# Kernel tuning notes

Hardware: AMD Instinct MI355X
Metric: run time of the kernel (lower is better)

Reference implementation:

```python
import jax, jax.numpy as jnp
import numpy as np

USER_NUM = 200000
ITEM_NUM = 100000
EMB = 64
N_LAYERS = 2
NE_S = 3200000
NE_R = 3200000


def setup_inputs() -> dict:
    key = jax.random.key(0)
    ks = jax.random.split(key, 10)
    scale = 1.0 / np.sqrt(EMB)
    user_emb = jax.random.normal(ks[0], (USER_NUM, EMB), jnp.float32) * scale
    item_emb = jax.random.normal(ks[1], (ITEM_NUM, EMB), jnp.float32) * scale
    # torch Linear weight is [out_features, in_features] = [EMB, 2*EMB]
    W = jax.random.normal(ks[2], (N_LAYERS, EMB, 2 * EMB), jnp.float32) * (1.0 / np.sqrt(2 * EMB))
    b = jnp.zeros((N_LAYERS, EMB), jnp.float32)
    s_rows = jax.random.randint(ks[3], (NE_S,), 0, USER_NUM, jnp.int32)
    s_cols = jax.random.randint(ks[4], (NE_S,), 0, USER_NUM, jnp.int32)
    s_vals = jax.random.uniform(ks[5], (NE_S,), jnp.float32) / 16.0  # ~row-normalized
    r_rows = jax.random.randint(ks[6], (NE_R,), 0, USER_NUM, jnp.int32)
    r_cols = jax.random.randint(ks[7], (NE_R,), 0, ITEM_NUM, jnp.int32)
    r_vals = jax.random.uniform(ks[8], (NE_R,), jnp.float32) / 16.0
    return {"user_emb": user_emb, "item_emb": item_emb, "W": W, "b": b,
            "s_rows": s_rows, "s_cols": s_cols, "s_vals": s_vals,
            "r_rows": r_rows, "r_cols": r_cols, "r_vals": r_vals}


def _spmm(rows, cols, vals, X, n_rows):
    # COO sparse [n_rows, n_cols] @ dense X[n_cols, d]
    return jax.ops.segment_sum(vals[:, None] * X[cols], rows, num_segments=n_rows)


def reference(user_emb, item_emb, W, b, s_rows, s_cols, s_vals, r_rows, r_cols, r_vals):
    U = user_emb
    V = item_emb
    for i in range(N_LAYERS):
        agg = _spmm(s_rows, s_cols, s_vals, U, USER_NUM)      # [U, EMB]
        h = jnp.concatenate([agg, U], axis=1)                 # [U, 2*EMB]
        U = jax.nn.relu(h @ W[i].T + b[i])                    # [U, EMB]
    user_all = U + _spmm(r_rows, r_cols, r_vals, V, USER_NUM)
    item_all = V
    return (user_all, item_all)
```

## Files before the change

kernel.cpp:

```cpp
#include <hip/hip_runtime.h>

#define USER_NUM 200000
#define ITEM_NUM 100000
#define EMB 64

#define SCAN_T 256
#define SCAN_E 8
#define SCAN_TILE (SCAN_T * SCAN_E)

__global__ __launch_bounds__(256) void hist_kernel(
    const int* __restrict__ rows, int nnz, int* __restrict__ cnt)
{
    int e = blockIdx.x * 256 + threadIdx.x;
    if (e >= nnz) return;
    atomicAdd(&cnt[rows[e]], 1);
}

__global__ __launch_bounds__(SCAN_T) void block_sum_kernel(
    const int* __restrict__ cnt, int n, int* __restrict__ partials)
{
    __shared__ int sm[SCAN_T];
    int tid = threadIdx.x;
    int base = blockIdx.x * SCAN_TILE + tid * SCAN_E;
    int s = 0;
    #pragma unroll
    for (int j = 0; j < SCAN_E; ++j) {
        int i = base + j;
        if (i < n) s += cnt[i];
    }
    sm[tid] = s; __syncthreads();
    for (int off = SCAN_T / 2; off > 0; off >>= 1) {
        if (tid < off) sm[tid] += sm[tid + off];
        __syncthreads();
    }
    if (tid == 0) partials[blockIdx.x] = sm[0];
}

__global__ __launch_bounds__(SCAN_T) void scan_partials_kernel(
    int* __restrict__ partials, int nblocks)
{
    __shared__ int sm[SCAN_T];
    int tid = threadIdx.x;
    int v = (tid < nblocks) ? partials[tid] : 0;
    sm[tid] = v; __syncthreads();
    for (int off = 1; off < SCAN_T; off <<= 1) {
        int a = (tid >= off) ? sm[tid - off] : 0;
        __syncthreads();
        sm[tid] += a;
        __syncthreads();
    }
    if (tid < nblocks) partials[tid] = sm[tid] - v;
}

__global__ __launch_bounds__(SCAN_T) void scan_tile_kernel(
    const int* __restrict__ cnt, int n, const int* __restrict__ partials,
    int* __restrict__ row_ptr)
{
    __shared__ int sm[SCAN_T];
    int tid = threadIdx.x;
    int base = blockIdx.x * SCAN_TILE + tid * SCAN_E;
    int local[SCAN_E];
    int s = 0;
    #pragma unroll
    for (int j = 0; j < SCAN_E; ++j) {
        int i = base + j;
        local[j] = (i < n) ? cnt[i] : 0;
        s += local[j];
    }
    sm[tid] = s; __syncthreads();
    for (int off = 1; off < SCAN_T; off <<= 1) {
        int a = (tid >= off) ? sm[tid - off] : 0;
        __syncthreads();
        sm[tid] += a;
        __syncthreads();
    }
    int run = partials[blockIdx.x] + (sm[tid] - s);
    #pragma unroll
    for (int j = 0; j < SCAN_E; ++j) {
        int i = base + j;
        if (i < n) row_ptr[i] = run;
        run += local[j];
        if (i == n - 1) row_ptr[n] = run;
    }
}

__global__ __launch_bounds__(256) void scatter_kernel(
    const int* __restrict__ rows, const int* __restrict__ cols,
    const float* __restrict__ vals, int nnz,
    const int* __restrict__ row_ptr, int* __restrict__ cursor,
    int* __restrict__ ecols, float* __restrict__ evals)
{
    int e = blockIdx.x * 256 + threadIdx.x;
    if (e >= nnz) return;
    int r = rows[e];
    int p = row_ptr[r] + atomicAdd(&cursor[r], 1);
    ecols[p] = cols[e];
    evals[p] = vals[e];
}

__global__ __launch_bounds__(256) void spmm_csr_kernel(
    const int* __restrict__ row_ptr, const int* __restrict__ ecols,
    const float* __restrict__ evals, const float* __restrict__ X,
    const float* __restrict__ addin, float* __restrict__ out, int n_rows)
{
    int gid = blockIdx.x * 256 + threadIdx.x;
    int row = gid >> 6;
    int lane = gid & 63;
    if (row >= n_rows) return;
    int beg = row_ptr[row], end = row_ptr[row + 1];
    float acc = addin ? addin[(size_t)row * EMB + lane] : 0.0f;
    int i = beg;
    for (; i + 1 < end; i += 2) {
        int   c0 = ecols[i],   c1 = ecols[i + 1];
        float v0 = evals[i],   v1 = evals[i + 1];
        float x0 = X[(size_t)c0 * EMB + lane];
        float x1 = X[(size_t)c1 * EMB + lane];
        acc = fmaf(v0, x0, acc);
        acc = fmaf(v1, x1, acc);
    }
    if (i < end) {
        int c = ecols[i];
        acc = fmaf(evals[i], X[(size_t)c * EMB + lane], acc);
    }
    out[(size_t)row * EMB + lane] = acc;
}

__global__ __launch_bounds__(256) void spmm_atomic_kernel(
    const int* __restrict__ rows, const int* __restrict__ cols,
    const float* __restrict__ vals, const float* __restrict__ X,
    float* __restrict__ out, int nnz)
{
    int t = blockIdx.x * 256 + threadIdx.x;
    int e = t >> 4;
    if (e >= nnz) return;
    int q = (t & 15) << 2;
    int r = rows[e];
    int c = cols[e];
    float v = vals[e];
    float4 x = *reinterpret_cast<const float4*>(X + (size_t)c * EMB + q);
    float* o = out + (size_t)r * EMB + q;
    atomicAdd(o + 0, v * x.x);
    atomicAdd(o + 1, v * x.y);
    atomicAdd(o + 2, v * x.z);
    atomicAdd(o + 3, v * x.w);
}

__global__ __launch_bounds__(256) void dense_relu_kernel(
    const float* __restrict__ agg, const float* __restrict__ Uin,
    const float* __restrict__ W,
    const float* __restrict__ bias,
    float* __restrict__ Uout, int nrows)
{
    int u = blockIdx.x * 256 + threadIdx.x;
    if (u >= nrows) return;

    float acc[EMB];
    #pragma unroll
    for (int k = 0; k < EMB; ++k) acc[k] = bias[k];

    const float* rowA = agg + (size_t)u * EMB;
    const float* rowU = Uin + (size_t)u * EMB;

    #pragma unroll 1
    for (int jc = 0; jc < 8; ++jc) {
        const float* src = (jc < 4) ? (rowA + jc * 16) : (rowU + (jc - 4) * 16);
        float4 h0 = reinterpret_cast<const float4*>(src)[0];
        float4 h1 = reinterpret_cast<const float4*>(src)[1];
        float4 h2 = reinterpret_cast<const float4*>(src)[2];
        float4 h3 = reinterpret_cast<const float4*>(src)[3];
        float hbuf[16] = {h0.x,h0.y,h0.z,h0.w, h1.x,h1.y,h1.z,h1.w,
                          h2.x,h2.y,h2.z,h2.w, h3.x,h3.y,h3.z,h3.w};
        const float* wbase = W + jc * 16;
        #pragma unroll
        for (int k = 0; k < EMB; ++k) {
            const float* wr = wbase + (size_t)k * 128;
            #pragma unroll
            for (int j = 0; j < 16; ++j)
                acc[k] = fmaf(hbuf[j], wr[j], acc[k]);
        }
    }

    float* orow = Uout + (size_t)u * EMB;
    #pragma unroll
    for (int kc = 0; kc < 16; ++kc) {
        float4 o;
        o.x = fmaxf(acc[kc*4+0], 0.f);
        o.y = fmaxf(acc[kc*4+1], 0.f);
        o.z = fmaxf(acc[kc*4+2], 0.f);
        o.w = fmaxf(acc[kc*4+3], 0.f);
        reinterpret_cast<float4*>(orow)[kc] = o;
    }
}

static void build_csr(const int* rows, const int* cols, const float* vals,
                      int nnz, int n_rows, int* cnt, int* partials,
                      int* row_ptr, int* ecols, float* evals,
                      hipStream_t stream)
{
    int nScan = (n_rows + SCAN_TILE - 1) / SCAN_TILE;
    hipMemsetAsync(cnt, 0, (size_t)n_rows * sizeof(int), stream);
    hist_kernel<<<(nnz + 255) / 256, 256, 0, stream>>>(rows, nnz, cnt);
    block_sum_kernel<<<nScan, SCAN_T, 0, stream>>>(cnt, n_rows, partials);
    scan_partials_kernel<<<1, SCAN_T, 0, stream>>>(partials, nScan);
    scan_tile_kernel<<<nScan, SCAN_T, 0, stream>>>(cnt, n_rows, partials, row_ptr);
    hipMemsetAsync(cnt, 0, (size_t)n_rows * sizeof(int), stream);
    scatter_kernel<<<(nnz + 255) / 256, 256, 0, stream>>>(rows, cols, vals, nnz,
                                                          row_ptr, cnt, ecols, evals);
}

extern "C" void kernel_launch(void* const* d_in, const int* in_sizes, int n_in,
                              void* d_out, int out_size, void* d_ws, size_t ws_size,
                              hipStream_t stream) {
    const float* user_emb = (const float*)d_in[0];
    const float* item_emb = (const float*)d_in[1];
    const float* W        = (const float*)d_in[2];
    const float* b        = (const float*)d_in[3];
    const int*   s_rows   = (const int*)d_in[4];
    const int*   s_cols   = (const int*)d_in[5];
    const float* s_vals   = (const float*)d_in[6];
    const int*   r_rows   = (const int*)d_in[7];
    const int*   r_cols   = (const int*)d_in[8];
    const float* r_vals   = (const float*)d_in[9];

    int ne_s = in_sizes[4];
    int ne_r = in_sizes[7];

    float* out      = (float*)d_out;
    float* user_out = out;
    float* item_out = out + (size_t)USER_NUM * EMB;

    char* w = (char*)d_ws;
    float* agg      = (float*)w;  w += (size_t)USER_NUM * EMB * 4;
    int*   s_rowptr = (int*)w;    w += (size_t)(USER_NUM + 1) * 4;
    int*   r_rowptr = (int*)w;    w += (size_t)(USER_NUM + 1) * 4;
    int*   cnt      = (int*)w;    w += (size_t)USER_NUM * 4;
    int*   partials = (int*)w;    w += 256 * 4;
    int*   s_ecols  = (int*)w;    w += (size_t)ne_s * 4;
    float* s_evals  = (float*)w;  w += (size_t)ne_s * 4;
    int*   r_ecols  = (int*)w;    w += (size_t)ne_r * 4;
    float* r_evals  = (float*)w;  w += (size_t)ne_r * 4;
    size_t needed = (size_t)(w - (char*)d_ws);

    size_t aggBytes = (size_t)USER_NUM * EMB * sizeof(float);
    int denseBlocks = (USER_NUM + 255) / 256;
    int spmmBlocks  = (USER_NUM * 64 + 255) / 256;

    if (ws_size >= needed) {
        build_csr(s_rows, s_cols, s_vals, ne_s, USER_NUM,
                  cnt, partials, s_rowptr, s_ecols, s_evals, stream);
        build_csr(r_rows, r_cols, r_vals, ne_r, USER_NUM,
                  cnt, partials, r_rowptr, r_ecols, r_evals, stream);

        spmm_csr_kernel<<<spmmBlocks, 256, 0, stream>>>(
            s_rowptr, s_ecols, s_evals, user_emb, nullptr, agg, USER_NUM);
        dense_relu_kernel<<<denseBlocks, 256, 0, stream>>>(
            agg, user_emb, W, b, user_out, USER_NUM);

        spmm_csr_kernel<<<spmmBlocks, 256, 0, stream>>>(
            s_rowptr, s_ecols, s_evals, user_out, nullptr, agg, USER_NUM);
        dense_relu_kernel<<<denseBlocks, 256, 0, stream>>>(
            agg, user_out, W + 64 * 128, b + 64, user_out, USER_NUM);

        spmm_csr_kernel<<<spmmBlocks, 256, 0, stream>>>(
            r_rowptr, r_ecols, r_evals, item_emb, user_out, user_out, USER_NUM);
    } else {
        int spmmBlocksS = (ne_s * 16 + 255) / 256;
        int spmmBlocksR = (ne_r * 16 + 255) / 256;
        hipMemsetAsync(agg, 0, aggBytes, stream);
        spmm_atomic_kernel<<<spmmBlocksS, 256, 0, stream>>>(s_rows, s_cols, s_vals,
                                                            user_emb, agg, ne_s);
        dense_relu_kernel<<<denseBlocks, 256, 0, stream>>>(agg, user_emb, W, b,
                                                           user_out, USER_NUM);
        hipMemsetAsync(agg, 0, aggBytes, stream);
        spmm_atomic_kernel<<<spmmBlocksS, 256, 0, stream>>>(s_rows, s_cols, s_vals,
                                                            user_out, agg, ne_s);
        dense_relu_kernel<<<denseBlocks, 256, 0, stream>>>(agg, user_out,
                                                           W + 64 * 128, b + 64,
                                                           user_out, USER_NUM);
        spmm_atomic_kernel<<<spmmBlocksR, 256, 0, stream>>>(r_rows, r_cols, r_vals,
                                                            item_emb, user_out, ne_r);
    }

    hipMemcpyAsync(item_out, item_emb, (size_t)ITEM_NUM * EMB * sizeof(float),
                   hipMemcpyDeviceToDevice, stream);
}
```

Measured before the change: 1.920 ms.

## Interleave CSR col/val pairs, unroll SpMM, and stage W in LDS for dense

Column and value arrays are packed into a single int2 array, so scatter does one 8-byte store and SpMM one 8-byte load per edge. The SpMM inner loop is unrolled by four to keep more gathers in flight. The scan kernel now seeds the cursor with row offsets, which removes a memset and a row_ptr read in scatter. The dense ReLU layer copies W and the bias into shared memory and has each thread process two rows with a fixed grid of 512 blocks, so weights are reused from LDS instead of global memory. The cost is much higher register pressure from 128 accumulators per thread.

```diff
diff --git a/kernel.cpp b/kernel.cpp
--- a/kernel.cpp
+++ b/kernel.cpp
@@ -54,7 +54,7 @@
 
 __global__ __launch_bounds__(SCAN_T) void scan_tile_kernel(
     const int* __restrict__ cnt, int n, const int* __restrict__ partials,
-    int* __restrict__ row_ptr)
+    int* __restrict__ row_ptr, int* __restrict__ cursor)
 {
     __shared__ int sm[SCAN_T];
     int tid = threadIdx.x;
@@ -78,7 +78,7 @@
     #pragma unroll
     for (int j = 0; j < SCAN_E; ++j) {
         int i = base + j;
-        if (i < n) row_ptr[i] = run;
+        if (i < n) { row_ptr[i] = run; cursor[i] = run; }
         run += local[j];
         if (i == n - 1) row_ptr[n] = run;
     }
@@ -87,21 +87,19 @@
 __global__ __launch_bounds__(256) void scatter_kernel(
     const int* __restrict__ rows, const int* __restrict__ cols,
     const float* __restrict__ vals, int nnz,
-    const int* __restrict__ row_ptr, int* __restrict__ cursor,
-    int* __restrict__ ecols, float* __restrict__ evals)
+    int* __restrict__ cursor, int2* __restrict__ epairs)
 {
     int e = blockIdx.x * 256 + threadIdx.x;
     if (e >= nnz) return;
     int r = rows[e];
-    int p = row_ptr[r] + atomicAdd(&cursor[r], 1);
-    ecols[p] = cols[e];
-    evals[p] = vals[e];
+    int p = atomicAdd(&cursor[r], 1);
+    epairs[p] = make_int2(cols[e], __float_as_int(vals[e]));
 }
 
 __global__ __launch_bounds__(256) void spmm_csr_kernel(
-    const int* __restrict__ row_ptr, const int* __restrict__ ecols,
-    const float* __restrict__ evals, const float* __restrict__ X,
-    const float* __restrict__ addin, float* __restrict__ out, int n_rows)
+    const int* __restrict__ row_ptr, const int2* __restrict__ epairs,
+    const float* __restrict__ X, const float* __restrict__ addin,
+    float* __restrict__ out, int n_rows)
 {
     int gid = blockIdx.x * 256 + threadIdx.x;
     int row = gid >> 6;
@@ -110,17 +108,20 @@
     int beg = row_ptr[row], end = row_ptr[row + 1];
     float acc = addin ? addin[(size_t)row * EMB + lane] : 0.0f;
     int i = beg;
-    for (; i + 1 < end; i += 2) {
-        int   c0 = ecols[i],   c1 = ecols[i + 1];
-        float v0 = evals[i],   v1 = evals[i + 1];
-        float x0 = X[(size_t)c0 * EMB + lane];
-        float x1 = X[(size_t)c1 * EMB + lane];
-        acc = fmaf(v0, x0, acc);
-        acc = fmaf(v1, x1, acc);
-    }
-    if (i < end) {
-        int c = ecols[i];
-        acc = fmaf(evals[i], X[(size_t)c * EMB + lane], acc);
+    for (; i + 4 <= end; i += 4) {
+        int2 e0 = epairs[i], e1 = epairs[i+1], e2 = epairs[i+2], e3 = epairs[i+3];
+        float x0 = X[(size_t)e0.x * EMB + lane];
+        float x1 = X[(size_t)e1.x * EMB + lane];
+        float x2 = X[(size_t)e2.x * EMB + lane];
+        float x3 = X[(size_t)e3.x * EMB + lane];
+        acc = fmaf(__int_as_float(e0.y), x0, acc);
+        acc = fmaf(__int_as_float(e1.y), x1, acc);
+        acc = fmaf(__int_as_float(e2.y), x2, acc);
+        acc = fmaf(__int_as_float(e3.y), x3, acc);
+    }
+    for (; i < end; ++i) {
+        int2 e = epairs[i];
+        acc = fmaf(__int_as_float(e.y), X[(size_t)e.x * EMB + lane], acc);
     }
     out[(size_t)row * EMB + lane] = acc;
 }
@@ -145,67 +146,104 @@
     atomicAdd(o + 3, v * x.w);
 }
 
-__global__ __launch_bounds__(256) void dense_relu_kernel(
+#define DENSE_BLOCKS 512
+#define DENSE_SPAN (DENSE_BLOCKS * 256)
+
+__global__ __launch_bounds__(256, 2) void dense_relu_kernel(
     const float* __restrict__ agg, const float* __restrict__ Uin,
     const float* __restrict__ W,
     const float* __restrict__ bias,
     float* __restrict__ Uout, int nrows)
 {
-    int u = blockIdx.x * 256 + threadIdx.x;
-    if (u >= nrows) return;
-
-    float acc[EMB];
-    #pragma unroll
-    for (int k = 0; k < EMB; ++k) acc[k] = bias[k];
-
-    const float* rowA = agg + (size_t)u * EMB;
-    const float* rowU = Uin + (size_t)u * EMB;
+    __shared__ float Wl[64 * 128 + 64];
+    int tid = threadIdx.x;
+    #pragma unroll
+    for (int i = 0; i < 8; ++i) {
+        int idx = tid + i * 256;
+        reinterpret_cast<float4*>(Wl)[idx] = reinterpret_cast<const float4*>(W)[idx];
+    }
+    if (tid < 64) Wl[8192 + tid] = bias[tid];
+    __syncthreads();
+
+    int gid = blockIdx.x * 256 + tid;
+    int u0 = gid;
+    int u1 = gid + DENSE_SPAN;
+    bool ok1 = (u1 < nrows);
+    if (u0 >= nrows) return;
+
+    float acc[2][EMB];
+    #pragma unroll
+    for (int k = 0; k < EMB; ++k) {
+        float bv = Wl[8192 + k];
+        acc[0][k] = bv;
+        acc[1][k] = bv;
+    }
 
     #pragma unroll 1
-    for (int jc = 0; jc < 8; ++jc) {
-        const float* src = (jc < 4) ? (rowA + jc * 16) : (rowU + (jc - 4) * 16);
-        float4 h0 = reinterpret_cast<const float4*>(src)[0];
-        float4 h1 = reinterpret_cast<const float4*>(src)[1];
-        float4 h2 = reinterpret_cast<const float4*>(src)[2];
-        float4 h3 = reinterpret_cast<const float4*>(src)[3];
-        float hbuf[16] = {h0.x,h0.y,h0.z,h0.w, h1.x,h1.y,h1.z,h1.w,
-                          h2.x,h2.y,h2.z,h2.w, h3.x,h3.y,h3.z,h3.w};
-        const float* wbase = W + jc * 16;
+    for (int half = 0; half < 2; ++half) {
+        const float* __restrict__ src = half ? Uin : agg;
+        const float4* r0 = reinterpret_cast<const float4*>(src + (size_t)u0 * EMB);
+        const float4* r1 = ok1 ? reinterpret_cast<const float4*>(src + (size_t)u1 * EMB)
+                               : r0;
+        #pragma unroll 1
+        for (int jq = 0; jq < 16; ++jq) {
+            float4 h0 = r0[jq];
+            float4 h1 = r1[jq];
+            #pragma unroll
+            for (int k = 0; k < EMB; ++k) {
+                float4 wv = *reinterpret_cast<const float4*>(
+                    Wl + k * 128 + half * 64 + jq * 4);
+                acc[0][k] = fmaf(h0.x, wv.x, acc[0][k]);
+                acc[0][k] = fmaf(h0.y, wv.y, acc[0][k]);
+                acc[0][k] = fmaf(h0.z, wv.z, acc[0][k]);
+                acc[0][k] = fmaf(h0.w, wv.w, acc[0][k]);
+                acc[1][k] = fmaf(h1.x, wv.x, acc[1][k]);
+                acc[1][k] = fmaf(h1.y, wv.y, acc[1][k]);
+                acc[1][k] = fmaf(h1.z, wv.z, acc[1][k]);
+                acc[1][k] = fmaf(h1.w, wv.w, acc[1][k]);
+            }
+        }
+    }
+
+    {
+        float* orow = Uout + (size_t)u0 * EMB;
         #pragma unroll
-        for (int k = 0; k < EMB; ++k) {
-            const float* wr = wbase + (size_t)k * 128;
-            #pragma unroll
-            for (int j = 0; j < 16; ++j)
-                acc[k] = fmaf(hbuf[j], wr[j], acc[k]);
+        for (int q = 0; q < 16; ++q) {
+            float4 o;
+            o.x = fmaxf(acc[0][q*4+0], 0.f);
+            o.y = fmaxf(acc[0][q*4+1], 0.f);
+            o.z = fmaxf(acc[0][q*4+2], 0.f);
+            o.w = fmaxf(acc[0][q*4+3], 0.f);
+            reinterpret_cast<float4*>(orow)[q] = o;
         }
     }
-
-    float* orow = Uout + (size_t)u * EMB;
-    #pragma unroll
-    for (int kc = 0; kc < 16; ++kc) {
-        float4 o;
-        o.x = fmaxf(acc[kc*4+0], 0.f);
-        o.y = fmaxf(acc[kc*4+1], 0.f);
-        o.z = fmaxf(acc[kc*4+2], 0.f);
-        o.w = fmaxf(acc[kc*4+3], 0.f);
-        reinterpret_cast<float4*>(orow)[kc] = o;
+    if (ok1) {
+        float* orow = Uout + (size_t)u1 * EMB;
+        #pragma unroll
+        for (int q = 0; q < 16; ++q) {
+            float4 o;
+            o.x = fmaxf(acc[1][q*4+0], 0.f);
+            o.y = fmaxf(acc[1][q*4+1], 0.f);
+            o.z = fmaxf(acc[1][q*4+2], 0.f);
+            o.w = fmaxf(acc[1][q*4+3], 0.f);
+            reinterpret_cast<float4*>(orow)[q] = o;
+        }
     }
 }
 
 static void build_csr(const int* rows, const int* cols, const float* vals,
                       int nnz, int n_rows, int* cnt, int* partials,
-                      int* row_ptr, int* ecols, float* evals,
-                      hipStream_t stream)
+                      int* row_ptr, int2* epairs, hipStream_t stream)
 {
     int nScan = (n_rows + SCAN_TILE - 1) / SCAN_TILE;
     hipMemsetAsync(cnt, 0, (size_t)n_rows * sizeof(int), stream);
     hist_kernel<<<(nnz + 255) / 256, 256, 0, stream>>>(rows, nnz, cnt);
     block_sum_kernel<<<nScan, SCAN_T, 0, stream>>>(cnt, n_rows, partials);
     scan_partials_kernel<<<1, SCAN_T, 0, stream>>>(partials, nScan);
-    scan_tile_kernel<<<nScan, SCAN_T, 0, stream>>>(cnt, n_rows, partials, row_ptr);
-    hipMemsetAsync(cnt, 0, (size_t)n_rows * sizeof(int), stream);
+    scan_tile_kernel<<<nScan, SCAN_T, 0, stream>>>(cnt, n_rows, partials,
+                                                   row_ptr, cnt);
     scatter_kernel<<<(nnz + 255) / 256, 256, 0, stream>>>(rows, cols, vals, nnz,
-                                                          row_ptr, cnt, ecols, evals);
+                                                          cnt, epairs);
 }
 
 extern "C" void kernel_launch(void* const* d_in, const int* in_sizes, int n_in,
@@ -235,48 +273,45 @@
     int*   r_rowptr = (int*)w;    w += (size_t)(USER_NUM + 1) * 4;
     int*   cnt      = (int*)w;    w += (size_t)USER_NUM * 4;
     int*   partials = (int*)w;    w += 256 * 4;
-    int*   s_ecols  = (int*)w;    w += (size_t)ne_s * 4;
-    float* s_evals  = (float*)w;  w += (size_t)ne_s * 4;
-    int*   r_ecols  = (int*)w;    w += (size_t)ne_r * 4;
-    float* r_evals  = (float*)w;  w += (size_t)ne_r * 4;
+    int2*  s_epairs = (int2*)w;   w += (size_t)ne_s * 8;
+    int2*  r_epairs = (int2*)w;   w += (size_t)ne_r * 8;
     size_t needed = (size_t)(w - (char*)d_ws);
 
     size_t aggBytes = (size_t)USER_NUM * EMB * sizeof(float);
-    int denseBlocks = (USER_NUM + 255) / 256;
     int spmmBlocks  = (USER_NUM * 64 + 255) / 256;
 
     if (ws_size >= needed) {
         build_csr(s_rows, s_cols, s_vals, ne_s, USER_NUM,
-                  cnt, partials, s_rowptr, s_ecols, s_evals, stream);
+                  cnt, partials, s_rowptr, s_epairs, stream);
         build_csr(r_rows, r_cols, r_vals, ne_r, USER_NUM,
-                  cnt, partials, r_rowptr, r_ecols, r_evals, stream);
+                  cnt, partials, r_rowptr, r_epairs, stream);
 
         spmm_csr_kernel<<<spmmBlocks, 256, 0, stream>>>(
-            s_rowptr, s_ecols, s_evals, user_emb, nullptr, agg, USER_NUM);
-        dense_relu_kernel<<<denseBlocks, 256, 0, stream>>>(
+            s_rowptr, s_epairs, user_emb, nullptr, agg, USER_NUM);
+        dense_relu_kernel<<<DENSE_BLOCKS, 256, 0, stream>>>(
             agg, user_emb, W, b, user_out, USER_NUM);
 
         spmm_csr_kernel<<<spmmBlocks, 256, 0, stream>>>(
-            s_rowptr, s_ecols, s_evals, user_out, nullptr, agg, USER_NUM);
-        dense_relu_kernel<<<denseBlocks, 256, 0, stream>>>(
+            s_rowptr, s_epairs, user_out, nullptr, agg, USER_NUM);
+        dense_relu_kernel<<<DENSE_BLOCKS, 256, 0, stream>>>(
             agg, user_out, W + 64 * 128, b + 64, user_out, USER_NUM);
 
         spmm_csr_kernel<<<spmmBlocks, 256, 0, stream>>>(
-            r_rowptr, r_ecols, r_evals, item_emb, user_out, user_out, USER_NUM);
+            r_rowptr, r_epairs, item_emb, user_out, user_out, USER_NUM);
     } else {
         int spmmBlocksS = (ne_s * 16 + 255) / 256;
         int spmmBlocksR = (ne_r * 16 + 255) / 256;
         hipMemsetAsync(agg, 0, aggBytes, stream);
         spmm_atomic_kernel<<<spmmBlocksS, 256, 0, stream>>>(s_rows, s_cols, s_vals,
                                                             user_emb, agg, ne_s);
-        dense_relu_kernel<<<denseBlocks, 256, 0, stream>>>(agg, user_emb, W, b,
-                                                           user_out, USER_NUM);
+        dense_relu_kernel<<<DENSE_BLOCKS, 256, 0, stream>>>(agg, user_emb, W, b,
+                                                            user_out, USER_NUM);
         hipMemsetAsync(agg, 0, aggBytes, stream);
         spmm_atomic_kernel<<<spmmBlocksS, 256, 0, stream>>>(s_rows, s_cols, s_vals,
                                                             user_out, agg, ne_s);
-        dense_relu_kernel<<<denseBlocks, 256, 0, stream>>>(agg, user_out,
-                                                           W + 64 * 128, b + 64,
-                                                           user_out, USER_NUM);
+        dense_relu_kernel<<<DENSE_BLOCKS, 256, 0, stream>>>(agg, user_out,
+                                                            W + 64 * 128, b + 64,
+                                                            user_out, USER_NUM);
         spmm_atomic_kernel<<<spmmBlocksR, 256, 0, stream>>>(r_rows, r_cols, r_vals,
                                                             item_emb, user_out, ne_r);
     }
```

Result: faster. 1.538 ms (-19.9%).
